# Kernel optimization log

Measured on AMD Instinct MI355X. Metric: run time of the kernel, lower is better.

## Reference

```python
import jax, jax.numpy as jnp
import numpy as np

B, S, D, E, H = 2, 1024, 1024, 8, 3584
Z_COEF = 1e-3
LOAD_COEF = 1e-3


def setup_inputs() -> dict:
    key = jax.random.key(0)
    k = jax.random.split(key, 5)
    x = jax.random.normal(k[0], (B, S, D), dtype=jnp.float32)
    Wr = jax.random.normal(k[1], (E, D), dtype=jnp.float32) / np.sqrt(D)   # router: Linear(D, E) weight [out,in]
    W1 = jax.random.normal(k[2], (E, H, D), dtype=jnp.float32) / np.sqrt(D)  # per-expert w1 [out=H,in=D]
    W2 = jax.random.normal(k[3], (E, H, D), dtype=jnp.float32) / np.sqrt(D)  # per-expert w2
    W3 = jax.random.normal(k[4], (E, D, H), dtype=jnp.float32) / np.sqrt(H)  # per-expert w3 [out=D,in=H]
    return {"x": x, "Wr": Wr, "W1": W1, "W2": W2, "W3": W3}


def reference(x, Wr, W1, W2, W3):
    b, s, d = x.shape
    e = Wr.shape[0]
    # Router
    router_logits = jnp.einsum('bsd,ed->bse', x, Wr)            # [B,S,E]
    probs = jax.nn.softmax(router_logits, axis=-1)
    topk_probs, topk_idx = jax.lax.top_k(probs, 1)              # top_k = 1 (see notes)
    # Dense one-hot dispatch (faithful to original einsum dispatch)
    flat_x = x.reshape(-1, d)                                   # [N,D]
    flat_idx = topk_idx.reshape(-1)                             # [N]
    mask = jax.nn.one_hot(flat_idx, e, dtype=x.dtype)           # [N,E]
    xin = jnp.einsum('ne,nd->end', mask, flat_x)                # [E,N,D] masked expert inputs
    # All experts over all tokens (SwiGLU), batched over E
    h = jax.nn.silu(jnp.einsum('end,ehd->enh', xin, W1)) * jnp.einsum('end,ehd->enh', xin, W2)
    out_e = jnp.einsum('enh,edh->end', h, W3)                   # [E,N,D]
    # Combine with the 0/1 mask (original does NOT weight by topk_probs)
    out = jnp.einsum('end,ne->nd', out_e, mask).reshape(b, s, d)
    # dropout p=0 -> identity
    # Aux losses
    z_loss = jnp.mean(jax.nn.logsumexp(router_logits, axis=-1)) ** 2
    expert_load = probs.sum(axis=0)                             # [S,E] (sum over dim 0, as in torch)
    load_loss = (jnp.std(expert_load, ddof=1) / jnp.mean(expert_load)) ** 2
    aux_loss = Z_COEF * z_loss + LOAD_COEF * load_loss
    return out, aux_loss
```

## Files before the change

### kernel.cpp

```cpp
#include <hip/hip_runtime.h>
#include <hip/hip_bf16.h>
#include <math.h>


#define NS 1024
#define ND 1024
#define NE 8
#define NH 3584
#define NTOK 2048
#define LDK 72

typedef float f32x4 __attribute__((ext_vector_type(4)));
typedef __bf16 bf16x8 __attribute__((ext_vector_type(8)));
typedef unsigned short u16x4 __attribute__((ext_vector_type(4)));
typedef unsigned int u32x4 __attribute__((ext_vector_type(4)));

__device__ __forceinline__ u16x4 cvt4(f32x4 v) {
  u16x4 r;
  r[0] = __builtin_bit_cast(unsigned short, (__bf16)v[0]);
  r[1] = __builtin_bit_cast(unsigned short, (__bf16)v[1]);
  r[2] = __builtin_bit_cast(unsigned short, (__bf16)v[2]);
  r[3] = __builtin_bit_cast(unsigned short, (__bf16)v[3]);
  return r;
}

__device__ __forceinline__ void gl_lds16(const void* g, void* l) {
  __builtin_amdgcn_global_load_lds(
      (const __attribute__((address_space(1))) unsigned int*)g,
      (__attribute__((address_space(3))) unsigned int*)l, 16, 0, 0);
}

__global__ __launch_bounds__(256) void convert_x(
    const float* __restrict__ x, unsigned short* __restrict__ xb)
{
  size_t i = ((size_t)blockIdx.x * 256 + threadIdx.x) * 4;
  f32x4 v = *(const f32x4*)(x + i);
  *(u16x4*)(xb + i) = cvt4(v);
}

__global__ __launch_bounds__(256) void router_kernel(
    const float* __restrict__ x, const float* __restrict__ Wr,
    float* __restrict__ probs, float* __restrict__ lse,
    int* __restrict__ counts, int* __restrict__ expert_of)
{
  int n = blockIdx.x;
  int t = threadIdx.x;
  const float* xr = x + (size_t)n * ND;
  float xv[4];
#pragma unroll
  for (int j = 0; j < 4; ++j) xv[j] = xr[t + j * 256];
  float p[NE];
#pragma unroll
  for (int e = 0; e < NE; ++e) p[e] = 0.f;
#pragma unroll
  for (int j = 0; j < 4; ++j) {
    int d = t + j * 256;
#pragma unroll
    for (int e = 0; e < NE; ++e) p[e] += xv[j] * Wr[e * ND + d];
  }
#pragma unroll
  for (int e = 0; e < NE; ++e) {
#pragma unroll
    for (int o = 32; o > 0; o >>= 1) p[e] += __shfl_down(p[e], o, 64);
  }
  __shared__ float red[4][NE];
  int wid = t >> 6, lane = t & 63;
  if (lane == 0) {
#pragma unroll
    for (int e = 0; e < NE; ++e) red[wid][e] = p[e];
  }
  __syncthreads();
  if (t == 0) {
    float lg[NE];
#pragma unroll
    for (int e = 0; e < NE; ++e) lg[e] = red[0][e] + red[1][e] + red[2][e] + red[3][e];
    float m = lg[0]; int arg = 0;
#pragma unroll
    for (int e = 1; e < NE; ++e) if (lg[e] > m) { m = lg[e]; arg = e; }
    float s = 0.f, ex[NE];
#pragma unroll
    for (int e = 0; e < NE; ++e) { ex[e] = expf(lg[e] - m); s += ex[e]; }
    float inv = 1.f / s;
#pragma unroll
    for (int e = 0; e < NE; ++e) probs[n * NE + e] = ex[e] * inv;
    lse[n] = m + logf(s);
    expert_of[n] = arg;
    atomicAdd(&counts[arg], 1);
  }
}

__global__ __launch_bounds__(256) void aux_offsets_kernel(
    const float* __restrict__ probs, const float* __restrict__ lse,
    const int* __restrict__ counts, int* __restrict__ offsets,
    int* __restrict__ cursors, float* __restrict__ out_aux)
{
  int t = threadIdx.x;
  float lsum = 0.f;
  for (int n = t; n < NTOK; n += 256) lsum += lse[n];
  float esum = 0.f, esq = 0.f;
  for (int i = t; i < NS * NE; i += 256) {
    float v = probs[i] + probs[NS * NE + i];
    esum += v; esq += v * v;
  }
  __shared__ float rb[3][4];
  int wid = t >> 6, lane = t & 63;
#pragma unroll
  for (int o = 32; o > 0; o >>= 1) {
    lsum += __shfl_down(lsum, o, 64);
    esum += __shfl_down(esum, o, 64);
    esq  += __shfl_down(esq, o, 64);
  }
  if (lane == 0) { rb[0][wid] = lsum; rb[1][wid] = esum; rb[2][wid] = esq; }
  __syncthreads();
  if (t == 0) {
    lsum = rb[0][0] + rb[0][1] + rb[0][2] + rb[0][3];
    esum = rb[1][0] + rb[1][1] + rb[1][2] + rb[1][3];
    esq  = rb[2][0] + rb[2][1] + rb[2][2] + rb[2][3];
    float zmean = lsum / (float)NTOK;
    float z_loss = zmean * zmean;
    const float nn = (float)(NS * NE);
    float mean = esum / nn;
    float var = (esq - esum * esum / nn) / (nn - 1.0f);
    float load_loss = var / (mean * mean);
    out_aux[0] = 1e-3f * z_loss + 1e-3f * load_loss;
    int off = 0;
#pragma unroll
    for (int e = 0; e < NE; ++e) { offsets[e] = off; cursors[e] = off; off += counts[e]; }
    offsets[NE] = off;
  }
}

__global__ __launch_bounds__(256) void scatter_kernel(
    const int* __restrict__ expert_of, int* __restrict__ cursors,
    int* __restrict__ token_list)
{
  int n = blockIdx.x * 256 + threadIdx.x;
  int e = expert_of[n];
  int p = atomicAdd(&cursors[e], 1);
  token_list[p] = n;
}

__global__ __launch_bounds__(256) void moe_gemm12(
    const unsigned short* __restrict__ xb, const float* __restrict__ W1f,
    const float* __restrict__ W2f, const int* __restrict__ offsets,
    const int* __restrict__ token_list, unsigned short* __restrict__ h)
{
  int e = blockIdx.z;
  int base = offsets[e], cnt = offsets[e + 1] - base;
  int m0 = blockIdx.y * 128;
  if (m0 >= cnt) return;
  int n0 = blockIdx.x * 64;
  const float* B1 = W1f + (size_t)e * ((size_t)NH * ND) + (size_t)n0 * ND;
  const float* B2 = W2f + (size_t)e * ((size_t)NH * ND) + (size_t)n0 * ND;

  __shared__ __align__(16) unsigned short As[2][128][64];
  __shared__ __align__(16) unsigned short B1s[2][64][LDK];
  __shared__ __align__(16) unsigned short B2s[2][64][LDK];
  __shared__ int rowtok[128];

  int t = threadIdx.x;
  if (t < 128) {
    int mc = m0 + t; if (mc > cnt - 1) mc = cnt - 1;
    rowtok[t] = token_list[base + mc];
  }
  __syncthreads();

  int lane = t & 63, wid = t >> 6;

  const char* aSrc[4];
  {
    int l8 = lane >> 3, blk = lane & 7;
    int sblk = blk ^ l8;
#pragma unroll
    for (int i = 0; i < 4; ++i) {
      int R = wid * 32 + i * 8 + l8;
      aSrc[i] = (const char*)(xb + (size_t)rowtok[R] * ND + sblk * 8);
    }
  }
  unsigned aldsOff = wid * 4096;

  auto stageA = [&](int buf, int ks) {
    char* dst = (char*)&As[buf][0][0] + aldsOff;
#pragma unroll
    for (int i = 0; i < 4; ++i)
      gl_lds16(aSrc[i] + ks * 128, dst + i * 1024);
  };

  int rsub = t >> 4;
  int c4 = (t & 15) * 4;
  const float* b1p = B1 + (size_t)rsub * ND + c4;
  const float* b2p = B2 + (size_t)rsub * ND + c4;

  f32x4 s0b1[4], s0b2[4], s1b1[4], s1b2[4];

  auto loadB_s0 = [&](int k0) {
#pragma unroll
    for (int rr = 0; rr < 4; ++rr) {
      s0b1[rr] = *(const f32x4*)(b1p + (size_t)rr * 16 * ND + k0);
      s0b2[rr] = *(const f32x4*)(b2p + (size_t)rr * 16 * ND + k0);
    }
  };
  auto loadB_s1 = [&](int k0) {
#pragma unroll
    for (int rr = 0; rr < 4; ++rr) {
      s1b1[rr] = *(const f32x4*)(b1p + (size_t)rr * 16 * ND + k0);
      s1b2[rr] = *(const f32x4*)(b2p + (size_t)rr * 16 * ND + k0);
    }
  };
  auto writeB_s0 = [&](int buf) {
#pragma unroll
    for (int rr = 0; rr < 4; ++rr) {
      *(u16x4*)&B1s[buf][rr * 16 + rsub][c4] = cvt4(s0b1[rr]);
      *(u16x4*)&B2s[buf][rr * 16 + rsub][c4] = cvt4(s0b2[rr]);
    }
  };
  auto writeB_s1 = [&](int buf) {
#pragma unroll
    for (int rr = 0; rr < 4; ++rr) {
      *(u16x4*)&B1s[buf][rr * 16 + rsub][c4] = cvt4(s1b1[rr]);
      *(u16x4*)&B2s[buf][rr * 16 + rsub][c4] = cvt4(s1b2[rr]);
    }
  };

  int wm = (wid >> 1) * 64;
  int wn = (wid & 1) * 32;
  int rl = lane & 15;
  int ksel8 = (lane >> 4) * 8;
  int xorf = rl & 7;

  f32x4 acc1[4][2] = {}, acc2[4][2] = {};

  auto mfma = [&](int buf) {
#pragma unroll
    for (int kk = 0; kk < 2; ++kk) {
      int klo = kk * 32 + ksel8;
      int g = (klo >> 3) ^ xorf;
      bf16x8 af[4], b1v[2], b2v[2];
#pragma unroll
      for (int i = 0; i < 4; ++i) {
        int row = wm + i * 16 + rl;
        af[i] = *(const bf16x8*)((const char*)&As[buf][0][0] + row * 128 + (g << 4));
      }
#pragma unroll
      for (int j = 0; j < 2; ++j) {
        b1v[j] = *(const bf16x8*)&B1s[buf][wn + j * 16 + rl][klo];
        b2v[j] = *(const bf16x8*)&B2s[buf][wn + j * 16 + rl][klo];
      }
#pragma unroll
      for (int i = 0; i < 4; ++i)
#pragma unroll
        for (int j = 0; j < 2; ++j) {
          acc1[i][j] = __builtin_amdgcn_mfma_f32_16x16x32_bf16(af[i], b1v[j], acc1[i][j], 0, 0, 0);
          acc2[i][j] = __builtin_amdgcn_mfma_f32_16x16x32_bf16(af[i], b2v[j], acc2[i][j], 0, 0, 0);
        }
    }
  };

  stageA(0, 0);
  loadB_s0(0);
  loadB_s1(64);
  writeB_s0(0);
  __syncthreads();

  const int NSTEP = ND / 64;
  for (int ks = 0; ks < NSTEP; ks += 2) {
    stageA(1, ks + 1);
    if (ks + 2 < NSTEP) loadB_s0((ks + 2) * 64);
    mfma(0);
    writeB_s1(1);
    __syncthreads();
    if (ks + 2 < NSTEP) stageA(0, ks + 2);
    if (ks + 3 < NSTEP) loadB_s1((ks + 3) * 64);
    mfma(1);
    if (ks + 2 < NSTEP) writeB_s0(0);
    __syncthreads();
  }

  int rq = lane >> 4;
#pragma unroll
  for (int i = 0; i < 4; ++i)
#pragma unroll
    for (int r = 0; r < 4; ++r) {
      int mrow = wm + i * 16 + rq * 4 + r;
      int m = m0 + mrow;
      if (m < cnt) {
#pragma unroll
        for (int j = 0; j < 2; ++j) {
          int col = n0 + wn + j * 16 + rl;
          float g1 = acc1[i][j][r], g2 = acc2[i][j][r];
          float hv = g1 / (1.f + expf(-g1)) * g2;
          h[(size_t)(base + m) * NH + col] = __builtin_bit_cast(unsigned short, (__bf16)hv);
        }
      }
    }
}

__global__ __launch_bounds__(256, 4) void moe_gemm3(
    const unsigned short* __restrict__ h, const float* __restrict__ W3f,
    const int* __restrict__ offsets, const int* __restrict__ token_list,
    float* __restrict__ out)
{
  int e = blockIdx.z;
  int base = offsets[e], cnt = offsets[e + 1] - base;
  int m0 = blockIdx.y * 128;
  if (m0 >= cnt) return;
  int n0 = (blockIdx.x >> 1) * 64;
  int kc = blockIdx.x & 1;
  const int KOFF = kc * (NH / 2);
  const float* B = W3f + (size_t)e * ((size_t)ND * NH) + (size_t)n0 * NH + KOFF;

  __shared__ __align__(16) unsigned short As[2][128][64];
  __shared__ __align__(16) unsigned short Bs[2][64][LDK];
  __shared__ int rowtok[128];

  int t = threadIdx.x;
  if (t < 128) {
    int mc = m0 + t; if (mc > cnt - 1) mc = cnt - 1;
    rowtok[t] = token_list[base + mc];
  }
  __syncthreads();

  int lane = t & 63, wid = t >> 6;

  const char* aSrc[4];
  {
    int l8 = lane >> 3, blk = lane & 7;
    int sblk = blk ^ l8;
#pragma unroll
    for (int i = 0; i < 4; ++i) {
      int R = wid * 32 + i * 8 + l8;
      int mc = m0 + R; if (mc > cnt - 1) mc = cnt - 1;
      aSrc[i] = (const char*)(h + (size_t)(base + mc) * NH + KOFF + sblk * 8);
    }
  }
  unsigned aldsOff = wid * 4096;

  auto stageA = [&](int buf, int ks) {
    char* dst = (char*)&As[buf][0][0] + aldsOff;
#pragma unroll
    for (int i = 0; i < 4; ++i)
      gl_lds16(aSrc[i] + ks * 128, dst + i * 1024);
  };

  int rsub = t >> 4;
  int c4 = (t & 15) * 4;
  const float* bp = B + (size_t)rsub * NH + c4;

  f32x4 s0b[4], s1b[4];
  auto loadB_s0 = [&](int k0) {
#pragma unroll
    for (int rr = 0; rr < 4; ++rr) s0b[rr] = *(const f32x4*)(bp + (size_t)rr * 16 * NH + k0);
  };
  auto loadB_s1 = [&](int k0) {
#pragma unroll
    for (int rr = 0; rr < 4; ++rr) s1b[rr] = *(const f32x4*)(bp + (size_t)rr * 16 * NH + k0);
  };
  auto writeB_s0 = [&](int buf) {
#pragma unroll
    for (int rr = 0; rr < 4; ++rr) *(u16x4*)&Bs[buf][rr * 16 + rsub][c4] = cvt4(s0b[rr]);
  };
  auto writeB_s1 = [&](int buf) {
#pragma unroll
    for (int rr = 0; rr < 4; ++rr) *(u16x4*)&Bs[buf][rr * 16 + rsub][c4] = cvt4(s1b[rr]);
  };

  int wm = (wid >> 1) * 64;
  int wn = (wid & 1) * 32;
  int rl = lane & 15;
  int ksel8 = (lane >> 4) * 8;
  int xorf = rl & 7;

  f32x4 acc[4][2] = {};

  auto mfma = [&](int buf) {
#pragma unroll
    for (int kk = 0; kk < 2; ++kk) {
      int klo = kk * 32 + ksel8;
      int g = (klo >> 3) ^ xorf;
      bf16x8 af[4], bv[2];
#pragma unroll
      for (int i = 0; i < 4; ++i) {
        int row = wm + i * 16 + rl;
        af[i] = *(const bf16x8*)((const char*)&As[buf][0][0] + row * 128 + (g << 4));
      }
#pragma unroll
      for (int j = 0; j < 2; ++j) bv[j] = *(const bf16x8*)&Bs[buf][wn + j * 16 + rl][klo];
#pragma unroll
      for (int i = 0; i < 4; ++i)
#pragma unroll
        for (int j = 0; j < 2; ++j)
          acc[i][j] = __builtin_amdgcn_mfma_f32_16x16x32_bf16(af[i], bv[j], acc[i][j], 0, 0, 0);
    }
  };

  stageA(0, 0);
  loadB_s0(0);
  loadB_s1(64);
  writeB_s0(0);
  __syncthreads();

  const int NSTEP = (NH / 2) / 64;
  for (int ks = 0; ks < NSTEP; ks += 2) {
    stageA(1, ks + 1);
    if (ks + 2 < NSTEP) loadB_s0((ks + 2) * 64);
    mfma(0);
    writeB_s1(1);
    __syncthreads();
    if (ks + 2 < NSTEP) stageA(0, ks + 2);
    if (ks + 3 < NSTEP) loadB_s1((ks + 3) * 64);
    mfma(1);
    if (ks + 2 < NSTEP) writeB_s0(0);
    __syncthreads();
  }

  int rq = lane >> 4;
#pragma unroll
  for (int i = 0; i < 4; ++i)
#pragma unroll
    for (int r = 0; r < 4; ++r) {
      int mrow = wm + i * 16 + rq * 4 + r;
      int m = m0 + mrow;
      if (m < cnt) {
        int tok = rowtok[mrow];
#pragma unroll
        for (int j = 0; j < 2; ++j) {
          int col = n0 + wn + j * 16 + rl;
          atomicAdd(&out[(size_t)tok * ND + col], acc[i][j][r]);
        }
      }
    }
}

extern "C" void kernel_launch(void* const* d_in, const int* in_sizes, int n_in,
                              void* d_out, int out_size, void* d_ws, size_t ws_size,
                              hipStream_t stream)
{
  (void)in_sizes; (void)n_in; (void)out_size; (void)ws_size;
  const float* x  = (const float*)d_in[0];
  const float* Wr = (const float*)d_in[1];
  const float* W1 = (const float*)d_in[2];
  const float* W2 = (const float*)d_in[3];
  const float* W3 = (const float*)d_in[4];
  float* out = (float*)d_out;

  char* w = (char*)d_ws;
  float* probs    = (float*)(w + 0);
  float* lse      = (float*)(w + 65536);
  int* counts     = (int*)(w + 73728);
  int* cursors    = (int*)(w + 73760);
  int* offsets    = (int*)(w + 73792);
  int* expert_of  = (int*)(w + 73856);
  int* token_list = (int*)(w + 82048);
  unsigned short* h  = (unsigned short*)(w + 131072);
  unsigned short* xb = (unsigned short*)(w + 131072 + 14680064);

  hipMemsetAsync(counts, 0, 32, stream);
  hipMemsetAsync(out, 0, (size_t)NTOK * ND * sizeof(float), stream);
  convert_x<<<NTOK * ND / (256 * 4), 256, 0, stream>>>(x, xb);
  router_kernel<<<NTOK, 256, 0, stream>>>(x, Wr, probs, lse, counts, expert_of);
  aux_offsets_kernel<<<1, 256, 0, stream>>>(probs, lse, counts, offsets, cursors,
                                            out + (size_t)NTOK * ND);
  scatter_kernel<<<NTOK / 256, 256, 0, stream>>>(expert_of, cursors, token_list);
  moe_gemm12<<<dim3(NH / 64, NTOK / 128, NE), 256, 0, stream>>>(
      xb, W1, W2, offsets, token_list, h);
  moe_gemm3<<<dim3((ND / 64) * 2, NTOK / 128, NE), 256, 0, stream>>>(
      h, W3, offsets, token_list, out);
}
```

Baseline: 210.3 us.

## Fuse x-to-bf16 conversion into router; relax barriers with partial vmcnt waits

```diff
diff --git a/kernel.cpp b/kernel.cpp
--- a/kernel.cpp
+++ b/kernel.cpp
@@ -14,6 +14,8 @@
 typedef __bf16 bf16x8 __attribute__((ext_vector_type(8)));
 typedef unsigned short u16x4 __attribute__((ext_vector_type(4)));
 typedef unsigned int u32x4 __attribute__((ext_vector_type(4)));
+
+#define CBAR(N) asm volatile("s_waitcnt vmcnt(" #N ") lgkmcnt(0)\n\ts_barrier" ::: "memory")
 
 __device__ __forceinline__ u16x4 cvt4(f32x4 v) {
   u16x4 r;
@@ -30,18 +32,11 @@
       (__attribute__((address_space(3))) unsigned int*)l, 16, 0, 0);
 }
 
-__global__ __launch_bounds__(256) void convert_x(
-    const float* __restrict__ x, unsigned short* __restrict__ xb)
-{
-  size_t i = ((size_t)blockIdx.x * 256 + threadIdx.x) * 4;
-  f32x4 v = *(const f32x4*)(x + i);
-  *(u16x4*)(xb + i) = cvt4(v);
-}
-
 __global__ __launch_bounds__(256) void router_kernel(
     const float* __restrict__ x, const float* __restrict__ Wr,
     float* __restrict__ probs, float* __restrict__ lse,
-    int* __restrict__ counts, int* __restrict__ expert_of)
+    int* __restrict__ counts, int* __restrict__ expert_of,
+    unsigned short* __restrict__ xb)
 {
   int n = blockIdx.x;
   int t = threadIdx.x;
@@ -49,6 +44,9 @@
   float xv[4];
 #pragma unroll
   for (int j = 0; j < 4; ++j) xv[j] = xr[t + j * 256];
+#pragma unroll
+  for (int j = 0; j < 4; ++j)
+    xb[(size_t)n * ND + t + j * 256] = __builtin_bit_cast(unsigned short, (__bf16)xv[j]);
   float p[NE];
 #pragma unroll
   for (int e = 0; e < NE; ++e) p[e] = 0.f;
@@ -184,6 +182,7 @@
 #pragma unroll
     for (int i = 0; i < 4; ++i)
       gl_lds16(aSrc[i] + ks * 128, dst + i * 1024);
+    __builtin_amdgcn_sched_barrier(0);
   };
 
   int rsub = t >> 4;
@@ -260,21 +259,26 @@
   loadB_s0(0);
   loadB_s1(64);
   writeB_s0(0);
-  __syncthreads();
+  CBAR(8);
 
   const int NSTEP = ND / 64;
-  for (int ks = 0; ks < NSTEP; ks += 2) {
+  for (int ks = 0; ks <= NSTEP - 4; ks += 2) {
     stageA(1, ks + 1);
-    if (ks + 2 < NSTEP) loadB_s0((ks + 2) * 64);
+    loadB_s0((ks + 2) * 64);
     mfma(0);
     writeB_s1(1);
-    __syncthreads();
-    if (ks + 2 < NSTEP) stageA(0, ks + 2);
-    if (ks + 3 < NSTEP) loadB_s1((ks + 3) * 64);
+    CBAR(8);
+    stageA(0, ks + 2);
+    loadB_s1((ks + 3) * 64);
     mfma(1);
-    if (ks + 2 < NSTEP) writeB_s0(0);
-    __syncthreads();
-  }
+    writeB_s0(0);
+    CBAR(8);
+  }
+  stageA(1, NSTEP - 1);
+  mfma(0);
+  writeB_s1(1);
+  __syncthreads();
+  mfma(1);
 
   int rq = lane >> 4;
 #pragma unroll
@@ -340,6 +344,7 @@
 #pragma unroll
     for (int i = 0; i < 4; ++i)
       gl_lds16(aSrc[i] + ks * 128, dst + i * 1024);
+    __builtin_amdgcn_sched_barrier(0);
   };
 
   int rsub = t >> 4;
@@ -397,21 +402,26 @@
   loadB_s0(0);
   loadB_s1(64);
   writeB_s0(0);
-  __syncthreads();
+  CBAR(4);
 
   const int NSTEP = (NH / 2) / 64;
-  for (int ks = 0; ks < NSTEP; ks += 2) {
+  for (int ks = 0; ks <= NSTEP - 4; ks += 2) {
     stageA(1, ks + 1);
-    if (ks + 2 < NSTEP) loadB_s0((ks + 2) * 64);
+    loadB_s0((ks + 2) * 64);
     mfma(0);
     writeB_s1(1);
-    __syncthreads();
-    if (ks + 2 < NSTEP) stageA(0, ks + 2);
-    if (ks + 3 < NSTEP) loadB_s1((ks + 3) * 64);
+    CBAR(4);
+    stageA(0, ks + 2);
+    loadB_s1((ks + 3) * 64);
     mfma(1);
-    if (ks + 2 < NSTEP) writeB_s0(0);
-    __syncthreads();
-  }
+    writeB_s0(0);
+    CBAR(4);
+  }
+  stageA(1, NSTEP - 1);
+  mfma(0);
+  writeB_s1(1);
+  __syncthreads();
+  mfma(1);
 
   int rq = lane >> 4;
 #pragma unroll
@@ -456,8 +466,7 @@
 
   hipMemsetAsync(counts, 0, 32, stream);
   hipMemsetAsync(out, 0, (size_t)NTOK * ND * sizeof(float), stream);
-  convert_x<<<NTOK * ND / (256 * 4), 256, 0, stream>>>(x, xb);
-  router_kernel<<<NTOK, 256, 0, stream>>>(x, Wr, probs, lse, counts, expert_of);
+  router_kernel<<<NTOK, 256, 0, stream>>>(x, Wr, probs, lse, counts, expert_of, xb);
   aux_offsets_kernel<<<1, 256, 0, stream>>>(probs, lse, counts, offsets, cursors,
                                             out + (size_t)NTOK * ND);
   scatter_kernel<<<NTOK / 256, 256, 0, stream>>>(expert_of, cursors, token_list);
```

Result: faster. 198.5 us (-5.6%).
